# Performance work log

Measured on AMD Instinct MI355X. Metric: run time of the kernel, lower is better.

## Reference

```python
import jax, jax.numpy as jnp
import numpy as np

EMBEDDINGS = 16
DENSE = 256
HEAD_SIZE = 64


def setup_inputs() -> dict:
    key = jax.random.key(0)
    ks = jax.random.split(key, 7)
    B, T = 4096, 100
    x = jax.random.normal(ks[0], (B, T, EMBEDDINGS), dtype=jnp.float32)
    s1 = EMBEDDINGS ** -0.5
    s2 = HEAD_SIZE ** -0.5
    # Linear weights stored as [in, out] (torch stores transposed; math identical)
    Wk = jax.random.uniform(ks[1], (EMBEDDINGS, HEAD_SIZE), jnp.float32, -s1, s1)
    Wq = jax.random.uniform(ks[2], (EMBEDDINGS, HEAD_SIZE), jnp.float32, -s1, s1)
    Wv = jax.random.uniform(ks[3], (EMBEDDINGS, HEAD_SIZE), jnp.float32, -s1, s1)
    Wdk = jax.random.uniform(ks[4], (HEAD_SIZE, DENSE), jnp.float32, -s2, s2)
    Wdq = jax.random.uniform(ks[5], (HEAD_SIZE, DENSE), jnp.float32, -s2, s2)
    Wdv = jax.random.uniform(ks[6], (HEAD_SIZE, DENSE), jnp.float32, -s2, s2)
    return {"x": x, "Wk": Wk, "Wq": Wq, "Wv": Wv, "Wdk": Wdk, "Wdq": Wdq, "Wdv": Wdv}


def reference(x, Wk, Wq, Wv, Wdk, Wdq, Wdv):
    B, T, C = x.shape
    # two chained bias-free projections per stream: [B,T,C] -> [B,T,H] -> [B,T,DENSE]
    k = (x @ Wk) @ Wdk
    q = (x @ Wq) @ Wdq
    v = (x @ Wv) @ Wdv
    # NOTE: original scales by C**-0.5 where C is the INPUT embedding dim (16)
    wei = jnp.einsum("btd,bsd->bts", q, k) * (C ** -0.5)  # [B,T,T]
    causal = jnp.tril(jnp.ones((T, T), dtype=bool))
    wei = jnp.where(causal, wei, -jnp.inf)
    wei = jax.nn.softmax(wei, axis=-1)
    # dropout omitted (eval-mode reference; training dropout is stochastic)
    out = wei @ v  # [B,T,DENSE]
    return out
```

## Files before the change

### kernel.cpp

```cpp
#include <hip/hip_runtime.h>

#define T_SEQ 100
#define C_EMB 16
#define DCOL  256


__global__ __launch_bounds__(256) void prep_kernel(
    const float* __restrict__ Wk, const float* __restrict__ Wq,
    const float* __restrict__ Wv, const float* __restrict__ Wdk,
    const float* __restrict__ Wdq, const float* __restrict__ Wdv,
    float* __restrict__ ws)
{
    __shared__ float WQL[16][260];
    __shared__ float WKL[16][260];
    const int tid = threadIdx.x;

    float aq[16], ak[16], av[16];
    #pragma unroll
    for (int i = 0; i < 16; ++i) { aq[i] = 0.f; ak[i] = 0.f; av[i] = 0.f; }
    for (int h = 0; h < 64; ++h) {
        const float wdq = Wdq[h*256 + tid];
        const float wdk = Wdk[h*256 + tid];
        const float wdv = Wdv[h*256 + tid];
        #pragma unroll
        for (int i = 0; i < 16; ++i) {
            aq[i] += Wq[i*64 + h] * wdq;
            ak[i] += Wk[i*64 + h] * wdk;
            av[i] += Wv[i*64 + h] * wdv;
        }
    }
    #pragma unroll
    for (int i = 0; i < 16; ++i) {
        WQL[i][tid] = aq[i];
        WKL[i][tid] = ak[i];
        ws[256 + i*256 + tid] = av[i];
    }
    __syncthreads();

    {
        const float scale = 0.25f * 1.4426950408889634f;
        const int k = tid >> 4;
        const int c = tid & 15;
        float acc = 0.f;
        for (int d4 = 0; d4 < 64; ++d4) {
            float4 a = *(const float4*)&WQL[k][4*d4];
            float4 b = *(const float4*)&WKL[c][4*d4];
            acc += a.x*b.x + a.y*b.y + a.z*b.z + a.w*b.w;
        }
        ws[k*16 + c] = acc * scale;
    }
}

__global__ __launch_bounds__(128) void attn_kernel(
    const float* __restrict__ x, const float* __restrict__ ws,
    float* __restrict__ out)
{
    __shared__ float Xs[T_SEQ * 16];
    __shared__ float Zs[T_SEQ * 16];

    const int b   = blockIdx.x;
    const int tid = threadIdx.x;
    const int t   = tid;
    const int wid = tid >> 6;

    const float* __restrict__ xb = x + (size_t)b * (T_SEQ * C_EMB);

    for (int i = tid; i < T_SEQ * 4; i += 128)
        ((float4*)Xs)[i] = ((const float4*)xb)[i];
    __syncthreads();

    const int tl = (t < T_SEQ) ? t : (T_SEQ - 1);
    float xt[16];
    #pragma unroll
    for (int i = 0; i < 4; ++i) {
        float4 q = ((const float4*)&Xs[tl * 16])[i];
        xt[4*i+0] = q.x; xt[4*i+1] = q.y; xt[4*i+2] = q.z; xt[4*i+3] = q.w;
    }

    float y[16];
    #pragma unroll
    for (int c = 0; c < 16; ++c) y[c] = 0.f;
    #pragma unroll
    for (int k = 0; k < 16; ++k) {
        const float xk = xt[k];
        #pragma unroll
        for (int c = 0; c < 16; ++c)
            y[c] += xk * ws[k*16 + c];
    }

    float z[16];
    #pragma unroll
    for (int c = 0; c < 16; ++c) z[c] = 0.f;
    float l = 0.f;

    const int smax = (wid == 0) ? 64 : T_SEQ;
    for (int s = 0; s < smax; ++s) {
        float sx[16];
        #pragma unroll
        for (int i = 0; i < 4; ++i) {
            float4 q = ((const float4*)&Xs[s * 16])[i];
            sx[4*i+0] = q.x; sx[4*i+1] = q.y; sx[4*i+2] = q.z; sx[4*i+3] = q.w;
        }
        float sc = 0.f;
        #pragma unroll
        for (int c = 0; c < 16; ++c) sc += y[c] * sx[c];
        float p = __builtin_amdgcn_exp2f(sc);
        p = (s <= t) ? p : 0.f;
        l += p;
        #pragma unroll
        for (int c = 0; c < 16; ++c) z[c] += p * sx[c];
    }

    if (t < T_SEQ) {
        const float li = __builtin_amdgcn_rcpf(l);
        #pragma unroll
        for (int i = 0; i < 4; ++i) {
            float4 q;
            q.x = z[4*i+0] * li; q.y = z[4*i+1] * li;
            q.z = z[4*i+2] * li; q.w = z[4*i+3] * li;
            ((float4*)&Zs[t * 16])[i] = q;
        }
    }
    __syncthreads();

    const int j = tid & 63;
    const float* __restrict__ WVp = ws + 256;
    float4 wv[16];
    #pragma unroll
    for (int c = 0; c < 16; ++c)
        wv[c] = *(const float4*)&WVp[c*256 + 4*j];

    float* __restrict__ outb = out + (size_t)b * (T_SEQ * DCOL);
    for (int tt = wid; tt < T_SEQ; tt += 2) {
        float zr[16];
        #pragma unroll
        for (int i = 0; i < 4; ++i) {
            float4 q = ((const float4*)&Zs[tt * 16])[i];
            zr[4*i+0] = q.x; zr[4*i+1] = q.y; zr[4*i+2] = q.z; zr[4*i+3] = q.w;
        }
        float4 acc = make_float4(0.f, 0.f, 0.f, 0.f);
        #pragma unroll
        for (int c = 0; c < 16; ++c) {
            acc.x += zr[c] * wv[c].x;
            acc.y += zr[c] * wv[c].y;
            acc.z += zr[c] * wv[c].z;
            acc.w += zr[c] * wv[c].w;
        }
        *(float4*)&outb[tt*256 + 4*j] = acc;
    }
}

extern "C" void kernel_launch(void* const* d_in, const int* in_sizes, int n_in,
                              void* d_out, int out_size, void* d_ws, size_t ws_size,
                              hipStream_t stream) {
    const float* x   = (const float*)d_in[0];
    const float* Wk  = (const float*)d_in[1];
    const float* Wq  = (const float*)d_in[2];
    const float* Wv  = (const float*)d_in[3];
    const float* Wdk = (const float*)d_in[4];
    const float* Wdq = (const float*)d_in[5];
    const float* Wdv = (const float*)d_in[6];
    float* out = (float*)d_out;
    float* ws  = (float*)d_ws;

    const int B = in_sizes[0] / (T_SEQ * C_EMB);

    prep_kernel<<<1, 256, 0, stream>>>(Wk, Wq, Wv, Wdk, Wdq, Wdv, ws);
    attn_kernel<<<B, 128, 0, stream>>>(x, ws, out);
}
```

Baseline: 561.4 us.

## Split attention into Z-computation kernel and separate grid-stride output projection kernel

Splits the fused attention kernel into two. The first computes the normalized 16-wide context Z per row and writes it to the workspace, falling back to the output buffer if the workspace is too small. The second is a persistent grid-stride kernel that projects Z through the 16x256 value matrix to produce the output. The split decouples the store-heavy projection from the latency-bound attention loop so the two phases can use different launch shapes, at the cost of an extra launch and a global round trip for Z. The inner loop is also rewritten with explicit fmaf and float4 operands.

```diff
diff --git a/kernel.cpp b/kernel.cpp
--- a/kernel.cpp
+++ b/kernel.cpp
@@ -51,12 +51,11 @@
     }
 }
 
-__global__ __launch_bounds__(128) void attn_kernel(
+__global__ __launch_bounds__(128) void attn_z_kernel(
     const float* __restrict__ x, const float* __restrict__ ws,
-    float* __restrict__ out)
+    float* __restrict__ Z, const int zstride)
 {
     __shared__ float Xs[T_SEQ * 16];
-    __shared__ float Zs[T_SEQ * 16];
 
     const int b   = blockIdx.x;
     const int tid = threadIdx.x;
@@ -85,68 +84,76 @@
         const float xk = xt[k];
         #pragma unroll
         for (int c = 0; c < 16; ++c)
-            y[c] += xk * ws[k*16 + c];
+            y[c] = fmaf(xk, ws[k*16 + c], y[c]);
     }
 
-    float z[16];
-    #pragma unroll
-    for (int c = 0; c < 16; ++c) z[c] = 0.f;
+    float4 z0 = {0,0,0,0}, z1 = {0,0,0,0}, z2 = {0,0,0,0}, z3 = {0,0,0,0};
     float l = 0.f;
 
     const int smax = (wid == 0) ? 64 : T_SEQ;
+    const float4* __restrict__ X4 = (const float4*)Xs;
     for (int s = 0; s < smax; ++s) {
-        float sx[16];
-        #pragma unroll
-        for (int i = 0; i < 4; ++i) {
-            float4 q = ((const float4*)&Xs[s * 16])[i];
-            sx[4*i+0] = q.x; sx[4*i+1] = q.y; sx[4*i+2] = q.z; sx[4*i+3] = q.w;
-        }
-        float sc = 0.f;
-        #pragma unroll
-        for (int c = 0; c < 16; ++c) sc += y[c] * sx[c];
+        float4 a0 = X4[s*4+0];
+        float4 a1 = X4[s*4+1];
+        float4 a2 = X4[s*4+2];
+        float4 a3 = X4[s*4+3];
+        float p0 = fmaf(y[ 3], a0.w, fmaf(y[ 2], a0.z, fmaf(y[ 1], a0.y, y[ 0]*a0.x)));
+        float p1 = fmaf(y[ 7], a1.w, fmaf(y[ 6], a1.z, fmaf(y[ 5], a1.y, y[ 4]*a1.x)));
+        float p2 = fmaf(y[11], a2.w, fmaf(y[10], a2.z, fmaf(y[ 9], a2.y, y[ 8]*a2.x)));
+        float p3 = fmaf(y[15], a3.w, fmaf(y[14], a3.z, fmaf(y[13], a3.y, y[12]*a3.x)));
+        float sc = (p0 + p1) + (p2 + p3);
         float p = __builtin_amdgcn_exp2f(sc);
         p = (s <= t) ? p : 0.f;
         l += p;
-        #pragma unroll
-        for (int c = 0; c < 16; ++c) z[c] += p * sx[c];
+        z0.x = fmaf(p, a0.x, z0.x); z0.y = fmaf(p, a0.y, z0.y);
+        z0.z = fmaf(p, a0.z, z0.z); z0.w = fmaf(p, a0.w, z0.w);
+        z1.x = fmaf(p, a1.x, z1.x); z1.y = fmaf(p, a1.y, z1.y);
+        z1.z = fmaf(p, a1.z, z1.z); z1.w = fmaf(p, a1.w, z1.w);
+        z2.x = fmaf(p, a2.x, z2.x); z2.y = fmaf(p, a2.y, z2.y);
+        z2.z = fmaf(p, a2.z, z2.z); z2.w = fmaf(p, a2.w, z2.w);
+        z3.x = fmaf(p, a3.x, z3.x); z3.y = fmaf(p, a3.y, z3.y);
+        z3.z = fmaf(p, a3.z, z3.z); z3.w = fmaf(p, a3.w, z3.w);
     }
 
     if (t < T_SEQ) {
         const float li = __builtin_amdgcn_rcpf(l);
-        #pragma unroll
-        for (int i = 0; i < 4; ++i) {
-            float4 q;
-            q.x = z[4*i+0] * li; q.y = z[4*i+1] * li;
-            q.z = z[4*i+2] * li; q.w = z[4*i+3] * li;
-            ((float4*)&Zs[t * 16])[i] = q;
-        }
+        float* __restrict__ zo = Z + ((size_t)b * T_SEQ + t) * zstride;
+        float4 o0 = {z0.x*li, z0.y*li, z0.z*li, z0.w*li};
+        float4 o1 = {z1.x*li, z1.y*li, z1.z*li, z1.w*li};
+        float4 o2 = {z2.x*li, z2.y*li, z2.z*li, z2.w*li};
+        float4 o3 = {z3.x*li, z3.y*li, z3.z*li, z3.w*li};
+        ((float4*)zo)[0] = o0; ((float4*)zo)[1] = o1;
+        ((float4*)zo)[2] = o2; ((float4*)zo)[3] = o3;
     }
-    __syncthreads();
+}
 
-    const int j = tid & 63;
+__global__ __launch_bounds__(256) void out_kernel(
+    const float* __restrict__ Z, const int zstride,
+    const float* __restrict__ ws, float* __restrict__ out, const int nrows)
+{
+    const int lane = threadIdx.x & 63;
+    const int gw   = (blockIdx.x << 2) + (threadIdx.x >> 6);
+    const int nw   = gridDim.x << 2;
+
     const float* __restrict__ WVp = ws + 256;
     float4 wv[16];
     #pragma unroll
     for (int c = 0; c < 16; ++c)
-        wv[c] = *(const float4*)&WVp[c*256 + 4*j];
+        wv[c] = *(const float4*)&WVp[c*256 + 4*lane];
 
-    float* __restrict__ outb = out + (size_t)b * (T_SEQ * DCOL);
-    for (int tt = wid; tt < T_SEQ; tt += 2) {
-        float zr[16];
-        #pragma unroll
-        for (int i = 0; i < 4; ++i) {
-            float4 q = ((const float4*)&Zs[tt * 16])[i];
-            zr[4*i+0] = q.x; zr[4*i+1] = q.y; zr[4*i+2] = q.z; zr[4*i+3] = q.w;
-        }
-        float4 acc = make_float4(0.f, 0.f, 0.f, 0.f);
+    for (int r = gw; r < nrows; r += nw) {
+        const int ru = __builtin_amdgcn_readfirstlane(r);
+        const float* __restrict__ zr = Z + (size_t)ru * zstride;
+        float4 acc = {0.f, 0.f, 0.f, 0.f};
         #pragma unroll
         for (int c = 0; c < 16; ++c) {
-            acc.x += zr[c] * wv[c].x;
-            acc.y += zr[c] * wv[c].y;
-            acc.z += zr[c] * wv[c].z;
-            acc.w += zr[c] * wv[c].w;
+            const float zc = zr[c];
+            acc.x = fmaf(zc, wv[c].x, acc.x);
+            acc.y = fmaf(zc, wv[c].y, acc.y);
+            acc.z = fmaf(zc, wv[c].z, acc.z);
+            acc.w = fmaf(zc, wv[c].w, acc.w);
         }
-        *(float4*)&outb[tt*256 + 4*j] = acc;
+        *(float4*)&out[(size_t)ru * DCOL + 4*lane] = acc;
     }
 }
 
@@ -163,8 +170,19 @@
     float* out = (float*)d_out;
     float* ws  = (float*)d_ws;
 
-    const int B = in_sizes[0] / (T_SEQ * C_EMB);
+    const int B     = in_sizes[0] / (T_SEQ * C_EMB);
+    const int nrows = B * T_SEQ;
 
     prep_kernel<<<1, 256, 0, stream>>>(Wk, Wq, Wv, Wdk, Wdq, Wdv, ws);
-    attn_kernel<<<B, 128, 0, stream>>>(x, ws, out);
+
+    const size_t zoff_floats  = 4352;
+    const size_t zneed_bytes  = (zoff_floats + (size_t)nrows * 16) * sizeof(float);
+    float* Z;
+    int zstride;
+    if (ws_size >= zneed_bytes) { Z = ws + zoff_floats; zstride = 16;   }
+    else                        { Z = out;              zstride = DCOL; }
+
+    attn_z_kernel<<<B, 128, 0, stream>>>(x, ws, Z, zstride);
+
+    out_kernel<<<2048, 256, 0, stream>>>(Z, zstride, ws, out, nrows);
 }
```

New measurement: 574.2 us. 1.02x slower.
